# Kernel optimization log

Hardware: AMD Instinct MI355X
Metric: run time of the kernel (lower is better)

Reference implementation:

```python
import jax, jax.numpy as jnp
import numpy as np
from jax import lax

N, C, K, M = 131072, 128, 27, 65536
EPS = 1e-5


def setup_inputs() -> dict:
    key = jax.random.key(0)
    ks = jax.random.split(key, 8)
    w_scale = 1.0 / np.sqrt(K * C)  # sane fan-in init for stacked kernel weights
    return {
        "x": jax.random.normal(ks[0], (N, C), jnp.float32),
        "W1": jax.random.normal(ks[1], (K, C, C), jnp.float32) * w_scale,
        "gamma1": jnp.ones((C,), jnp.float32),
        "beta1": jnp.zeros((C,), jnp.float32),
        "W2": jax.random.normal(ks[2], (K, C, C), jnp.float32) * w_scale,
        "gamma2": jnp.ones((C,), jnp.float32),
        "beta2": jnp.zeros((C,), jnp.float32),
        "map1_in": jax.random.randint(ks[3], (K, M), 0, N, jnp.int32),
        "map1_out": jax.random.randint(ks[4], (K, M), 0, N, jnp.int32),
        "map2_in": jax.random.randint(ks[5], (K, M), 0, N, jnp.int32),
        "map2_out": jax.random.randint(ks[6], (K, M), 0, N, jnp.int32),
    }


def sparse_conv(x, W, idx_in, idx_out):
    # gather-GEMM-scatter over K kernel offsets (Minkowski kernel map)
    def body(acc, kmap):
        w, ii, io = kmap                      # [C,C], [M], [M]
        contrib = x[ii] @ w                   # gather [M,C] then GEMM
        return acc.at[io].add(contrib), None  # scatter-add
    out, _ = lax.scan(body, jnp.zeros((x.shape[0], W.shape[-1]), x.dtype),
                      (W, idx_in, idx_out))
    return out


def batch_norm(x, gamma, beta):
    m = jnp.mean(x, axis=0)
    v = jnp.var(x, axis=0)
    return (x - m) * lax.rsqrt(v + EPS) * gamma + beta


def reference(x, W1, gamma1, beta1, W2, gamma2, beta2,
              map1_in, map1_out, map2_in, map2_out):
    residual = x
    out = sparse_conv(x, W1, map1_in, map1_out)
    out = jax.nn.elu(batch_norm(out, gamma1, beta1))
    out = sparse_conv(out, W2, map2_in, map2_out)
    out = batch_norm(out, gamma2, beta2) + residual
    return jax.nn.elu(out)
```

## Files before the change

kernel.cpp:

```cpp
#include <hip/hip_runtime.h>

typedef unsigned short u16;
typedef unsigned int u32;

#define NPTS 131072
#define CD 128
#define KOFF 27
#define MMAP 65536
#define LDAB 136
#define LDC 132

__device__ __forceinline__ u16 f2bf(float f) {
  u32 u = __float_as_uint(f);
  u32 r = (u + 0x7fffu + ((u >> 16) & 1u)) >> 16;
  return (u16)r;
}

typedef __attribute__((ext_vector_type(8))) short bf16x8;
typedef __attribute__((ext_vector_type(4))) float f32x4;

__global__ __launch_bounds__(256) void k_convert_x(const float* __restrict__ x,
                                                   u16* __restrict__ xb) {
  long i = ((long)blockIdx.x * 256 + threadIdx.x) * 8;
  float4 a = *(const float4*)(x + i);
  float4 b = *(const float4*)(x + i + 4);
  uint4 v;
  v.x = f2bf(a.x) | ((u32)f2bf(a.y) << 16);
  v.y = f2bf(a.z) | ((u32)f2bf(a.w) << 16);
  v.z = f2bf(b.x) | ((u32)f2bf(b.y) << 16);
  v.w = f2bf(b.z) | ((u32)f2bf(b.w) << 16);
  *(uint4*)(xb + i) = v;
}

__global__ __launch_bounds__(256) void k_convert_w(const float* __restrict__ W,
                                                   u16* __restrict__ Wb) {
  int idx = blockIdx.x * 256 + threadIdx.x;
  if (idx >= KOFF * 2048) return;
  int k = idx >> 11;
  int rem = idx & 2047;
  int co = rem >> 4;
  int cc = rem & 15;
  const float* ws = W + (long)k * (CD * CD) + (long)(cc * 8) * CD + co;
  u16 t[8];
#pragma unroll
  for (int j = 0; j < 8; ++j) t[j] = f2bf(ws[j * CD]);
  uint4 v;
  v.x = t[0] | ((u32)t[1] << 16);
  v.y = t[2] | ((u32)t[3] << 16);
  v.z = t[4] | ((u32)t[5] << 16);
  v.w = t[6] | ((u32)t[7] << 16);
  ((uint4*)Wb)[idx] = v;
}

__global__ __launch_bounds__(256) void k_hist(const int* __restrict__ mo,
                                              u32* __restrict__ hist) {
  int i = blockIdx.x * 256 + threadIdx.x;
  atomicAdd(&hist[mo[i]], 1u);
}

__global__ __launch_bounds__(256) void k_scanA(const u32* __restrict__ hist,
                                               u32* __restrict__ offs,
                                               u32* __restrict__ bsum) {
  __shared__ u32 sh[256];
  int t = threadIdx.x, b = blockIdx.x, i = b * 256 + t;
  u32 v = hist[i];
  u32 run = v;
  sh[t] = run;
  __syncthreads();
  for (int d = 1; d < 256; d <<= 1) {
    u32 y = (t >= d) ? sh[t - d] : 0u;
    __syncthreads();
    run += y;
    sh[t] = run;
    __syncthreads();
  }
  offs[i] = run - v;
  if (t == 255) bsum[b] = run;
}

__global__ __launch_bounds__(512) void k_scanB(u32* __restrict__ bsum) {
  __shared__ u32 sh[512];
  int t = threadIdx.x;
  u32 v = bsum[t];
  u32 run = v;
  sh[t] = run;
  __syncthreads();
  for (int d = 1; d < 512; d <<= 1) {
    u32 y = (t >= d) ? sh[t - d] : 0u;
    __syncthreads();
    run += y;
    sh[t] = run;
    __syncthreads();
  }
  bsum[t] = run - v;
}

__global__ __launch_bounds__(256) void k_scanC(u32* __restrict__ offs,
                                               const u32* __restrict__ bsum, u32 cnt) {
  int t = threadIdx.x, b = blockIdx.x, i = b * 256 + t;
  offs[i] += bsum[b];
  if (i == 0) offs[NPTS] = cnt;
}

__global__ __launch_bounds__(256) void k_rank(const int* __restrict__ mo,
                                              const u32* __restrict__ offs,
                                              u32* __restrict__ cur,
                                              u32* __restrict__ rank) {
  int i = blockIdx.x * 256 + threadIdx.x;
  int o = mo[i];
  rank[i] = offs[o] + atomicAdd(&cur[o], 1u);
}

__global__ __launch_bounds__(256) void k_gemm3(const u16* __restrict__ src,
                                               const u16* __restrict__ Wb,
                                               const int* __restrict__ mi,
                                               const u32* __restrict__ rank,
                                               u16* __restrict__ contrib,
                                               int kbase) {
  __shared__ u16 As[64 * LDAB];
  __shared__ u16 Bs[128 * LDAB];
  __shared__ u32 sin[64];
  __shared__ u32 srow[64];
  const int t = threadIdx.x;
  const int b = blockIdx.x;
  const int klocal = b >> 10;
  const int i0 = klocal * MMAP + (b & 1023) * 64;

  if (t < 64) {
    sin[t] = (u32)mi[i0 + t];
    srow[t] = rank[i0 + t];
  }
  const uint4* wsrc = (const uint4*)(Wb + (long)(kbase + klocal) * (CD * CD));
#pragma unroll
  for (int i = 0; i < 8; ++i) {
    int q = i * 256 + t;
    int co = q >> 4, cc = q & 15;
    *(uint4*)&Bs[co * LDAB + cc * 8] = wsrc[q];
  }
  __syncthreads();
#pragma unroll
  for (int i = 0; i < 4; ++i) {
    int q = i * 256 + t;
    int r = q >> 4, cc = q & 15;
    long row = sin[r];
    *(uint4*)&As[r * LDAB + cc * 8] = ((const uint4*)(src + row * CD))[cc];
  }
  __syncthreads();

  const int wave = t >> 6, lane = t & 63;
  const int lr = lane & 15, quad = lane >> 4;
  const int wm = (wave & 1) * 32;
  const int wn = (wave >> 1) * 64;
  f32x4 acc[2][4] = {};
#pragma unroll
  for (int kk = 0; kk < 4; ++kk) {
    bf16x8 a[2], bfr[4];
#pragma unroll
    for (int mt = 0; mt < 2; ++mt)
      a[mt] = *(const bf16x8*)&As[(wm + mt * 16 + lr) * LDAB + (kk * 4 + quad) * 8];
#pragma unroll
    for (int nt = 0; nt < 4; ++nt)
      bfr[nt] = *(const bf16x8*)&Bs[(wn + nt * 16 + lr) * LDAB + (kk * 4 + quad) * 8];
#pragma unroll
    for (int mt = 0; mt < 2; ++mt)
#pragma unroll
      for (int nt = 0; nt < 4; ++nt)
        acc[mt][nt] = __builtin_amdgcn_mfma_f32_16x16x32_bf16(a[mt], bfr[nt], acc[mt][nt], 0, 0, 0);
  }

  __syncthreads();
  u16* Cs = As;
#pragma unroll
  for (int mt = 0; mt < 2; ++mt)
#pragma unroll
    for (int v = 0; v < 4; ++v) {
      int slot = wm + mt * 16 + quad * 4 + v;
#pragma unroll
      for (int nt = 0; nt < 4; ++nt)
        Cs[slot * LDC + wn + nt * 16 + lr] = f2bf(acc[mt][nt][v]);
    }
  __syncthreads();
#pragma unroll
  for (int i = 0; i < 4; ++i) {
    int q = i * 256 + t;
    int r = q >> 4, cc = q & 15;
    size_t rk = srow[r];
    *(uint4*)(contrib + rk * CD + cc * 8) = *(const uint4*)&Cs[r * LDC + cc * 8];
  }
}

__global__ __launch_bounds__(256, 8) void k_segreduce4(const u16* __restrict__ contrib,
                                                       const u32* __restrict__ offs,
                                                       float* __restrict__ acc,
                                                       float* __restrict__ stats,
                                                       int first, int last) {
  __shared__ float sh[64][16];
  const int wave = threadIdx.x >> 6, lane = threadIdx.x & 63;
  const int W = blockIdx.x * 4 + wave;
  const int g = lane >> 4, sub = lane & 15;
  const int r0 = W * 16;
  u32 ld_off = offs[r0 + (lane < 17 ? lane : 16)];
  float sx[8], sx2[8];
#pragma unroll
  for (int j = 0; j < 8; ++j) {
    sx[j] = 0.f;
    sx2[j] = 0.f;
  }
  for (int b = 0; b < 4; ++b) {
    const int row = r0 + b * 4 + g;
    const u32 s0 = __shfl(ld_off, b * 4 + g);
    const u32 s1 = __shfl(ld_off, b * 4 + g + 1);
    const int len = (int)(s1 - s0);
    int ml = len;
    ml = max(ml, __shfl_xor(ml, 16));
    ml = max(ml, __shfl_xor(ml, 32));
    float v[8];
#pragma unroll
    for (int j = 0; j < 8; ++j) v[j] = 0.f;
    const u32* cp = (const u32*)(contrib + (size_t)s0 * CD) + sub * 4;
    for (int i = 0; i < ml; ++i) {
      if (i < len) {
        uint4 d = *(const uint4*)(cp + (size_t)i * 64);
        v[0] += __uint_as_float(d.x << 16);
        v[1] += __uint_as_float(d.x & 0xffff0000u);
        v[2] += __uint_as_float(d.y << 16);
        v[3] += __uint_as_float(d.y & 0xffff0000u);
        v[4] += __uint_as_float(d.z << 16);
        v[5] += __uint_as_float(d.z & 0xffff0000u);
        v[6] += __uint_as_float(d.w << 16);
        v[7] += __uint_as_float(d.w & 0xffff0000u);
      }
    }
    float4* ap = (float4*)(acc + (size_t)row * CD + sub * 8);
    if (!first) {
      float4 p0 = ap[0], p1 = ap[1];
      v[0] += p0.x;
      v[1] += p0.y;
      v[2] += p0.z;
      v[3] += p0.w;
      v[4] += p1.x;
      v[5] += p1.y;
      v[6] += p1.z;
      v[7] += p1.w;
    }
    ap[0] = make_float4(v[0], v[1], v[2], v[3]);
    ap[1] = make_float4(v[4], v[5], v[6], v[7]);
    if (last) {
#pragma unroll
      for (int j = 0; j < 8; ++j) {
        sx[j] += v[j];
        sx2[j] += v[j] * v[j];
      }
    }
  }
  if (last) {
#pragma unroll
    for (int j = 0; j < 8; ++j) {
      sx[j] += __shfl_xor(sx[j], 16);
      sx[j] += __shfl_xor(sx[j], 32);
      sx2[j] += __shfl_xor(sx2[j], 16);
      sx2[j] += __shfl_xor(sx2[j], 32);
    }
    if (lane < 16) {
#pragma unroll
      for (int j = 0; j < 8; ++j) {
        sh[wave * 16 + sub][j] = sx[j];
        sh[wave * 16 + sub][8 + j] = sx2[j];
      }
    }
    __syncthreads();
    if (threadIdx.x < 128) {
      int c = threadIdx.x, sb = c >> 3, j = c & 7;
      float a = sh[sb][j] + sh[16 + sb][j] + sh[32 + sb][j] + sh[48 + sb][j];
      float q = sh[sb][8 + j] + sh[16 + sb][8 + j] + sh[32 + sb][8 + j] + sh[48 + sb][8 + j];
      atomicAdd(&stats[c], a);
      atomicAdd(&stats[128 + c], q);
    }
  }
}

__global__ void k_finalize(const float* __restrict__ stats, const float* __restrict__ gamma,
                           const float* __restrict__ beta, float* __restrict__ scsh) {
  int c = threadIdx.x;
  float mean = stats[c] * (1.f / NPTS);
  float var = stats[128 + c] * (1.f / NPTS) - mean * mean;
  float sc = rsqrtf(var + 1e-5f) * gamma[c];
  scsh[c] = sc;
  scsh[128 + c] = beta[c] - mean * sc;
}

__device__ __forceinline__ float elu(float v) { return v > 0.f ? v : expf(v) - 1.f; }

__global__ __launch_bounds__(256) void k_apply_mid(const float* __restrict__ acc,
                                                   const float* __restrict__ scsh,
                                                   u16* __restrict__ y) {
  long i = ((long)blockIdx.x * 256 + threadIdx.x) * 4;
  int c = (int)(i & 127);
  float4 a = *(const float4*)(acc + i);
  float r0 = elu(a.x * scsh[c] + scsh[128 + c]);
  float r1 = elu(a.y * scsh[c + 1] + scsh[129 + c]);
  float r2 = elu(a.z * scsh[c + 2] + scsh[130 + c]);
  float r3 = elu(a.w * scsh[c + 3] + scsh[131 + c]);
  uint2 v;
  v.x = f2bf(r0) | ((u32)f2bf(r1) << 16);
  v.y = f2bf(r2) | ((u32)f2bf(r3) << 16);
  *(uint2*)(y + i) = v;
}

__global__ __launch_bounds__(256) void k_apply_final(const float* __restrict__ acc,
                                                     const float* __restrict__ scsh,
                                                     const float* __restrict__ x,
                                                     float* __restrict__ out) {
  long i = ((long)blockIdx.x * 256 + threadIdx.x) * 4;
  int c = (int)(i & 127);
  float4 a = *(const float4*)(acc + i);
  float4 rx = *(const float4*)(x + i);
  float4 o;
  o.x = elu(a.x * scsh[c] + scsh[128 + c] + rx.x);
  o.y = elu(a.y * scsh[c + 1] + scsh[129 + c] + rx.y);
  o.z = elu(a.z * scsh[c + 2] + scsh[130 + c] + rx.z);
  o.w = elu(a.w * scsh[c + 3] + scsh[131 + c] + rx.w);
  *(float4*)(out + i) = o;
}

extern "C" void kernel_launch(void* const* d_in, const int* in_sizes, int n_in,
                              void* d_out, int out_size, void* d_ws, size_t ws_size,
                              hipStream_t stream) {
  const float* x = (const float*)d_in[0];
  const float* W1 = (const float*)d_in[1];
  const float* g1 = (const float*)d_in[2];
  const float* b1 = (const float*)d_in[3];
  const float* W2 = (const float*)d_in[4];
  const float* g2 = (const float*)d_in[5];
  const float* b2 = (const float*)d_in[6];
  const int* m1i = (const int*)d_in[7];
  const int* m1o = (const int*)d_in[8];
  const int* m2i = (const int*)d_in[9];
  const int* m2o = (const int*)d_in[10];
  float* out = (float*)d_out;

  char* base = (char*)d_ws;
  size_t off = 0;
  auto alloc = [&](size_t bytes) -> void* {
    void* r = base + off;
    off = (off + bytes + 255) & ~(size_t)255;
    return r;
  };
  u16* xb = (u16*)alloc((size_t)NPTS * CD * 2);
  u16* Wb1 = (u16*)alloc((size_t)KOFF * CD * CD * 2);
  u16* Wb2 = (u16*)alloc((size_t)KOFF * CD * CD * 2);
  float* acc = (float*)alloc((size_t)NPTS * CD * 4);
  u32* hist = (u32*)alloc((size_t)NPTS * 4);
  u32* cur = (u32*)alloc((size_t)NPTS * 4);
  size_t msSize = (size_t)((char*)base + off - (char*)hist);
  u32* offs = (u32*)alloc(((size_t)NPTS + 1) * 4);
  float* stats = (float*)alloc(256 * 4);
  float* scsh = (float*)alloc(256 * 4);
  u32* bsum = (u32*)alloc(512 * 4);

  size_t per_k = (size_t)MMAP * CD * 2 + (size_t)MMAP * 4 + 512;
  size_t avail = (ws_size > off + 4096) ? (ws_size - off - 4096) : 0;
  int kcnt = (int)(avail / per_k);
  if (kcnt < 1) kcnt = 1;
  if (kcnt > KOFF) kcnt = KOFF;
  u32* rank = (u32*)alloc((size_t)kcnt * MMAP * 4);
  u16* contrib = (u16*)alloc((size_t)kcnt * MMAP * CD * 2);

  k_convert_x<<<(NPTS * CD) / 2048, 256, 0, stream>>>(x, xb);
  k_convert_w<<<(KOFF * 2048 + 255) / 256, 256, 0, stream>>>(W1, Wb1);
  k_convert_w<<<(KOFF * 2048 + 255) / 256, 256, 0, stream>>>(W2, Wb2);

  auto run_conv = [&](const u16* srcm, const u16* Wbm, const int* mi, const int* mo) {
    hipMemsetAsync(stats, 0, 1024, stream);
    for (int g0 = 0; g0 < KOFF; g0 += kcnt) {
      int kc = (KOFF - g0 < kcnt) ? (KOFF - g0) : kcnt;
      u32 cnt = (u32)kc * MMAP;
      hipMemsetAsync(hist, 0, msSize, stream);
      k_hist<<<cnt / 256, 256, 0, stream>>>(mo + (long)g0 * MMAP, hist);
      k_scanA<<<512, 256, 0, stream>>>(hist, offs, bsum);
      k_scanB<<<1, 512, 0, stream>>>(bsum);
      k_scanC<<<512, 256, 0, stream>>>(offs, bsum, cnt);
      k_rank<<<cnt / 256, 256, 0, stream>>>(mo + (long)g0 * MMAP, offs, cur, rank);
      k_gemm3<<<kc * 1024, 256, 0, stream>>>(srcm, Wbm, mi + (long)g0 * MMAP, rank, contrib, g0);
      k_segreduce4<<<2048, 256, 0, stream>>>(contrib, offs, acc, stats,
                                             g0 == 0 ? 1 : 0, (g0 + kc == KOFF) ? 1 : 0);
    }
  };

  run_conv(xb, Wb1, m1i, m1o);
  k_finalize<<<1, 128, 0, stream>>>(stats, g1, b1, scsh);
  k_apply_mid<<<(NPTS * CD) / 1024, 256, 0, stream>>>(acc, scsh, xb);

  run_conv(xb, Wb2, m2i, m2o);
  k_finalize<<<1, 128, 0, stream>>>(stats, g2, b2, scsh);
  k_apply_final<<<(NPTS * CD) / 1024, 256, 0, stream>>>(acc, scsh, x, out);
}
```

Baseline: 1.267 ms.

## Batch counting-sort setup across passes and split segment rows across wave quads

The histogram, scan and rank kernels now run once per convolution for all passes, using per-pass histogram, offset and cursor arrays, instead of once per pass. This removes many small launches and serial scan steps from the per-pass loop. The segmented reduction now has the four quads of a wave stride through the same row's segment and combine their partial sums with shuffles. Previously each quad handled its own row and waited on the longest row in its group, so this is meant to cut divergence and load imbalance. The cost is larger workspace for the per-pass metadata, which may lower kcnt, plus extra shuffles per row.

```diff
diff --git a/kernel.cpp b/kernel.cpp
--- a/kernel.cpp
+++ b/kernel.cpp
@@ -52,18 +52,20 @@
   ((uint4*)Wb)[idx] = v;
 }
 
-__global__ __launch_bounds__(256) void k_hist(const int* __restrict__ mo,
-                                              u32* __restrict__ hist) {
+__global__ __launch_bounds__(256) void k_hist2(const int* __restrict__ mo,
+                                               u32* __restrict__ hist, int bpp) {
+  int p = blockIdx.x / bpp;
   int i = blockIdx.x * 256 + threadIdx.x;
-  atomicAdd(&hist[mo[i]], 1u);
-}
-
-__global__ __launch_bounds__(256) void k_scanA(const u32* __restrict__ hist,
-                                               u32* __restrict__ offs,
-                                               u32* __restrict__ bsum) {
+  atomicAdd(&hist[(size_t)p * NPTS + mo[i]], 1u);
+}
+
+__global__ __launch_bounds__(256) void k_scanA2(const u32* __restrict__ hist,
+                                                u32* __restrict__ offs,
+                                                u32* __restrict__ bsum) {
   __shared__ u32 sh[256];
-  int t = threadIdx.x, b = blockIdx.x, i = b * 256 + t;
-  u32 v = hist[i];
+  int t = threadIdx.x, b = blockIdx.x;
+  int p = b >> 9, rblk = b & 511;
+  u32 v = hist[(size_t)p * NPTS + rblk * 256 + t];
   u32 run = v;
   sh[t] = run;
   __syncthreads();
@@ -74,14 +76,15 @@
     sh[t] = run;
     __syncthreads();
   }
-  offs[i] = run - v;
+  offs[(size_t)p * (NPTS + 1) + rblk * 256 + t] = run - v;
   if (t == 255) bsum[b] = run;
 }
 
-__global__ __launch_bounds__(512) void k_scanB(u32* __restrict__ bsum) {
+__global__ __launch_bounds__(512) void k_scanB2(u32* __restrict__ bsum) {
   __shared__ u32 sh[512];
   int t = threadIdx.x;
-  u32 v = bsum[t];
+  u32* bp = bsum + blockIdx.x * 512;
+  u32 v = bp[t];
   u32 run = v;
   sh[t] = run;
   __syncthreads();
@@ -92,23 +95,30 @@
     sh[t] = run;
     __syncthreads();
   }
-  bsum[t] = run - v;
-}
-
-__global__ __launch_bounds__(256) void k_scanC(u32* __restrict__ offs,
-                                               const u32* __restrict__ bsum, u32 cnt) {
-  int t = threadIdx.x, b = blockIdx.x, i = b * 256 + t;
-  offs[i] += bsum[b];
-  if (i == 0) offs[NPTS] = cnt;
-}
-
-__global__ __launch_bounds__(256) void k_rank(const int* __restrict__ mo,
-                                              const u32* __restrict__ offs,
-                                              u32* __restrict__ cur,
-                                              u32* __restrict__ rank) {
+  bp[t] = run - v;
+}
+
+__global__ __launch_bounds__(256) void k_scanC2(u32* __restrict__ offs,
+                                                const u32* __restrict__ bsum, int kcnt) {
+  int t = threadIdx.x, b = blockIdx.x;
+  int p = b >> 9, rblk = b & 511;
+  size_t base = (size_t)p * (NPTS + 1);
+  offs[base + rblk * 256 + t] += bsum[b];
+  if (rblk == 0 && t == 0) {
+    int kc = KOFF - p * kcnt;
+    if (kc > kcnt) kc = kcnt;
+    offs[base + NPTS] = (u32)kc * MMAP;
+  }
+}
+
+__global__ __launch_bounds__(256) void k_rank2(const int* __restrict__ mo,
+                                               const u32* __restrict__ offs,
+                                               u32* __restrict__ cur,
+                                               u32* __restrict__ rank, int bpp) {
+  int p = blockIdx.x / bpp;
   int i = blockIdx.x * 256 + threadIdx.x;
   int o = mo[i];
-  rank[i] = offs[o] + atomicAdd(&cur[o], 1u);
+  rank[i] = offs[(size_t)p * (NPTS + 1) + o] + atomicAdd(&cur[(size_t)p * NPTS + o], 1u);
 }
 
 __global__ __launch_bounds__(256) void k_gemm3(const u16* __restrict__ src,
@@ -189,92 +199,76 @@
   }
 }
 
-__global__ __launch_bounds__(256, 8) void k_segreduce4(const u16* __restrict__ contrib,
+__global__ __launch_bounds__(256, 8) void k_segreduce5(const u16* __restrict__ contrib,
                                                        const u32* __restrict__ offs,
                                                        float* __restrict__ acc,
                                                        float* __restrict__ stats,
                                                        int first, int last) {
-  __shared__ float sh[64][16];
   const int wave = threadIdx.x >> 6, lane = threadIdx.x & 63;
   const int W = blockIdx.x * 4 + wave;
-  const int g = lane >> 4, sub = lane & 15;
+  const int quad = lane >> 4, sub = lane & 15;
   const int r0 = W * 16;
   u32 ld_off = offs[r0 + (lane < 17 ? lane : 16)];
-  float sx[8], sx2[8];
-#pragma unroll
-  for (int j = 0; j < 8; ++j) {
-    sx[j] = 0.f;
-    sx2[j] = 0.f;
-  }
-  for (int b = 0; b < 4; ++b) {
-    const int row = r0 + b * 4 + g;
-    const u32 s0 = __shfl(ld_off, b * 4 + g);
-    const u32 s1 = __shfl(ld_off, b * 4 + g + 1);
-    const int len = (int)(s1 - s0);
-    int ml = len;
-    ml = max(ml, __shfl_xor(ml, 16));
-    ml = max(ml, __shfl_xor(ml, 32));
+  float s0a = 0.f, s1a = 0.f, q0a = 0.f, q1a = 0.f;
+#pragma unroll 2
+  for (int b = 0; b < 16; ++b) {
+    const int row = r0 + b;
+    const u32 e0 = __shfl(ld_off, b);
+    const u32 e1 = __shfl(ld_off, b + 1);
+    const int len = (int)(e1 - e0);
     float v[8];
 #pragma unroll
     for (int j = 0; j < 8; ++j) v[j] = 0.f;
-    const u32* cp = (const u32*)(contrib + (size_t)s0 * CD) + sub * 4;
-    for (int i = 0; i < ml; ++i) {
-      if (i < len) {
-        uint4 d = *(const uint4*)(cp + (size_t)i * 64);
-        v[0] += __uint_as_float(d.x << 16);
-        v[1] += __uint_as_float(d.x & 0xffff0000u);
-        v[2] += __uint_as_float(d.y << 16);
-        v[3] += __uint_as_float(d.y & 0xffff0000u);
-        v[4] += __uint_as_float(d.z << 16);
-        v[5] += __uint_as_float(d.z & 0xffff0000u);
-        v[6] += __uint_as_float(d.w << 16);
-        v[7] += __uint_as_float(d.w & 0xffff0000u);
-      }
-    }
-    float4* ap = (float4*)(acc + (size_t)row * CD + sub * 8);
+    const u32* cp = (const u32*)(contrib + (size_t)e0 * CD) + sub * 4;
+    for (int i = quad; i < len; i += 4) {
+      uint4 d = *(const uint4*)(cp + (size_t)i * 64);
+      v[0] += __uint_as_float(d.x << 16);
+      v[1] += __uint_as_float(d.x & 0xffff0000u);
+      v[2] += __uint_as_float(d.y << 16);
+      v[3] += __uint_as_float(d.y & 0xffff0000u);
+      v[4] += __uint_as_float(d.z << 16);
+      v[5] += __uint_as_float(d.z & 0xffff0000u);
+      v[6] += __uint_as_float(d.w << 16);
+      v[7] += __uint_as_float(d.w & 0xffff0000u);
+    }
+#pragma unroll
+    for (int j = 0; j < 8; ++j) {
+      v[j] += __shfl_xor(v[j], 16);
+      v[j] += __shfl_xor(v[j], 32);
+    }
+    float2* ap = (float2*)(acc + (size_t)row * CD) + (sub * 4 + quad);
+    float c0 = v[2 * quad], c1 = v[2 * quad + 1];
     if (!first) {
-      float4 p0 = ap[0], p1 = ap[1];
-      v[0] += p0.x;
-      v[1] += p0.y;
-      v[2] += p0.z;
-      v[3] += p0.w;
-      v[4] += p1.x;
-      v[5] += p1.y;
-      v[6] += p1.z;
-      v[7] += p1.w;
-    }
-    ap[0] = make_float4(v[0], v[1], v[2], v[3]);
-    ap[1] = make_float4(v[4], v[5], v[6], v[7]);
+      float2 pv = *ap;
+      c0 += pv.x;
+      c1 += pv.y;
+    }
+    *ap = make_float2(c0, c1);
     if (last) {
-#pragma unroll
-      for (int j = 0; j < 8; ++j) {
-        sx[j] += v[j];
-        sx2[j] += v[j] * v[j];
-      }
+      s0a += c0;
+      q0a += c0 * c0;
+      s1a += c1;
+      q1a += c1 * c1;
     }
   }
   if (last) {
-#pragma unroll
-    for (int j = 0; j < 8; ++j) {
-      sx[j] += __shfl_xor(sx[j], 16);
-      sx[j] += __shfl_xor(sx[j], 32);
-      sx2[j] += __shfl_xor(sx2[j], 16);
-      sx2[j] += __shfl_xor(sx2[j], 32);
-    }
-    if (lane < 16) {
-#pragma unroll
-      for (int j = 0; j < 8; ++j) {
-        sh[wave * 16 + sub][j] = sx[j];
-        sh[wave * 16 + sub][8 + j] = sx2[j];
-      }
-    }
+    __shared__ float sh[256][4];
+    sh[threadIdx.x][0] = s0a;
+    sh[threadIdx.x][1] = s1a;
+    sh[threadIdx.x][2] = q0a;
+    sh[threadIdx.x][3] = q1a;
     __syncthreads();
-    if (threadIdx.x < 128) {
-      int c = threadIdx.x, sb = c >> 3, j = c & 7;
-      float a = sh[sb][j] + sh[16 + sb][j] + sh[32 + sb][j] + sh[48 + sb][j];
-      float q = sh[sb][8 + j] + sh[16 + sb][8 + j] + sh[32 + sb][8 + j] + sh[48 + sb][8 + j];
-      atomicAdd(&stats[c], a);
-      atomicAdd(&stats[128 + c], q);
+    if (threadIdx.x < 64) {
+      int l = threadIdx.x;
+      int c = (l & 15) * 8 + (l >> 4) * 2;
+      float S0 = sh[l][0] + sh[64 + l][0] + sh[128 + l][0] + sh[192 + l][0];
+      float S1 = sh[l][1] + sh[64 + l][1] + sh[128 + l][1] + sh[192 + l][1];
+      float Q0 = sh[l][2] + sh[64 + l][2] + sh[128 + l][2] + sh[192 + l][2];
+      float Q1 = sh[l][3] + sh[64 + l][3] + sh[128 + l][3] + sh[192 + l][3];
+      atomicAdd(&stats[c], S0);
+      atomicAdd(&stats[c + 1], S1);
+      atomicAdd(&stats[128 + c], Q0);
+      atomicAdd(&stats[128 + c + 1], Q1);
     }
   }
 }
@@ -350,40 +344,51 @@
   u16* Wb1 = (u16*)alloc((size_t)KOFF * CD * CD * 2);
   u16* Wb2 = (u16*)alloc((size_t)KOFF * CD * CD * 2);
   float* acc = (float*)alloc((size_t)NPTS * CD * 4);
-  u32* hist = (u32*)alloc((size_t)NPTS * 4);
-  u32* cur = (u32*)alloc((size_t)NPTS * 4);
-  size_t msSize = (size_t)((char*)base + off - (char*)hist);
-  u32* offs = (u32*)alloc(((size_t)NPTS + 1) * 4);
   float* stats = (float*)alloc(256 * 4);
   float* scsh = (float*)alloc(256 * 4);
-  u32* bsum = (u32*)alloc(512 * 4);
-
-  size_t per_k = (size_t)MMAP * CD * 2 + (size_t)MMAP * 4 + 512;
-  size_t avail = (ws_size > off + 4096) ? (ws_size - off - 4096) : 0;
-  int kcnt = (int)(avail / per_k);
-  if (kcnt < 1) kcnt = 1;
-  if (kcnt > KOFF) kcnt = KOFF;
-  u32* rank = (u32*)alloc((size_t)kcnt * MMAP * 4);
+
+  int kcnt = 1, P = KOFF;
+  for (int kc = KOFF; kc >= 1; --kc) {
+    int Pp = (KOFF + kc - 1) / kc;
+    size_t need = off + 2 * (size_t)Pp * NPTS * 4 + 512
+                  + (size_t)Pp * (NPTS + 1) * 4 + 256
+                  + (size_t)Pp * 512 * 4 + 256
+                  + (size_t)KOFF * MMAP * 4 + 256
+                  + (size_t)kc * MMAP * CD * 2 + 4096;
+    if (need <= ws_size) {
+      kcnt = kc;
+      P = Pp;
+      break;
+    }
+  }
+  u32* hist = (u32*)alloc((size_t)P * NPTS * 4);
+  u32* cur = (u32*)alloc((size_t)P * NPTS * 4);
+  u32* offs = (u32*)alloc((size_t)P * (NPTS + 1) * 4);
+  u32* bsum = (u32*)alloc((size_t)P * 512 * 4);
+  u32* rank = (u32*)alloc((size_t)KOFF * MMAP * 4);
   u16* contrib = (u16*)alloc((size_t)kcnt * MMAP * CD * 2);
 
   k_convert_x<<<(NPTS * CD) / 2048, 256, 0, stream>>>(x, xb);
   k_convert_w<<<(KOFF * 2048 + 255) / 256, 256, 0, stream>>>(W1, Wb1);
   k_convert_w<<<(KOFF * 2048 + 255) / 256, 256, 0, stream>>>(W2, Wb2);
 
+  const int nb = (KOFF * MMAP) / 256;
+  const int bpp = kcnt * (MMAP / 256);
+
   auto run_conv = [&](const u16* srcm, const u16* Wbm, const int* mi, const int* mo) {
     hipMemsetAsync(stats, 0, 1024, stream);
-    for (int g0 = 0; g0 < KOFF; g0 += kcnt) {
-      int kc = (KOFF - g0 < kcnt) ? (KOFF - g0) : kcnt;
-      u32 cnt = (u32)kc * MMAP;
-      hipMemsetAsync(hist, 0, msSize, stream);
-      k_hist<<<cnt / 256, 256, 0, stream>>>(mo + (long)g0 * MMAP, hist);
-      k_scanA<<<512, 256, 0, stream>>>(hist, offs, bsum);
-      k_scanB<<<1, 512, 0, stream>>>(bsum);
-      k_scanC<<<512, 256, 0, stream>>>(offs, bsum, cnt);
-      k_rank<<<cnt / 256, 256, 0, stream>>>(mo + (long)g0 * MMAP, offs, cur, rank);
-      k_gemm3<<<kc * 1024, 256, 0, stream>>>(srcm, Wbm, mi + (long)g0 * MMAP, rank, contrib, g0);
-      k_segreduce4<<<2048, 256, 0, stream>>>(contrib, offs, acc, stats,
-                                             g0 == 0 ? 1 : 0, (g0 + kc == KOFF) ? 1 : 0);
+    hipMemsetAsync(hist, 0, 2 * (size_t)P * NPTS * 4, stream);
+    k_hist2<<<nb, 256, 0, stream>>>(mo, hist, bpp);
+    k_scanA2<<<512 * P, 256, 0, stream>>>(hist, offs, bsum);
+    k_scanB2<<<P, 512, 0, stream>>>(bsum);
+    k_scanC2<<<512 * P, 256, 0, stream>>>(offs, bsum, kcnt);
+    k_rank2<<<nb, 256, 0, stream>>>(mo, offs, cur, rank, bpp);
+    for (int p = 0; p < P; ++p) {
+      int kc = (KOFF - p * kcnt < kcnt) ? KOFF - p * kcnt : kcnt;
+      k_gemm3<<<kc * 1024, 256, 0, stream>>>(srcm, Wbm, mi + (long)p * kcnt * MMAP,
+                                             rank + (long)p * kcnt * MMAP, contrib, p * kcnt);
+      k_segreduce5<<<2048, 256, 0, stream>>>(contrib, offs + (size_t)p * (NPTS + 1), acc, stats,
+                                             p == 0 ? 1 : 0, p == P - 1 ? 1 : 0);
     }
   };
 
```

Result: slower. 1.335 ms (+5.4%).
